# Optimization experiments

Measured on AMD Instinct MI355X. Metric: run time of the kernel, lower is better.

Reference implementation:

```python
import jax, jax.numpy as jnp
import numpy as np

N = 20000
E = 640000
C_IN = 256
C_OUT = 256
K = 2
EPS = 1e-12


def setup_inputs() -> dict:
    key = jax.random.key(0)
    k1, k2, k3, k4, k5 = jax.random.split(key, 5)
    x = jax.random.normal(k1, (N, C_IN), dtype=jnp.float32)
    edge_index = jax.random.randint(k2, (2, E), 0, N, dtype=jnp.int64)
    edge_weights = jax.random.uniform(k3, (E,), dtype=jnp.float32)
    lin_w = jax.random.normal(k4, (C_OUT, C_IN), dtype=jnp.float32) / np.sqrt(C_IN)
    lin_b = jax.random.normal(k5, (C_OUT,), dtype=jnp.float32) * 0.01
    return {"x": x, "edge_index": edge_index, "edge_weights": edge_weights,
            "lin_w": lin_w, "lin_b": lin_b}


def reference(x, edge_index, edge_weights, lin_w, lin_b):
    row, col = edge_index[0], edge_index[1]  # source -> target

    # F.normalize(x, p=2, dim=-1)
    nrm = jnp.sqrt(jnp.sum(x * x, axis=-1, keepdims=True))
    x = x / jnp.maximum(nrm, EPS)

    # gcn_norm with add_self_loops=False (PyG): deg over target nodes
    deg = jax.ops.segment_sum(edge_weights, col, num_segments=N)
    deg_inv_sqrt = jnp.where(deg > 0, 1.0 / jnp.sqrt(deg), 0.0)
    norm = deg_inv_sqrt[row] * edge_weights * deg_inv_sqrt[col]  # [E]

    # K-hop propagation: out[col] += norm * x[row]
    for _ in range(K):
        msgs = norm[:, None] * x[row]                     # [E, C]
        x = jax.ops.segment_sum(msgs, col, num_segments=N)

    # Linear layer of SGConv
    return x @ lin_w.T + lin_b
```

## Files before the change

### kernel.cpp

```cpp
#include <hip/hip_runtime.h>
#include <hip/hip_bf16.h>

#define N_NODES 20000
#define N_EDGES 640000
#define C 256
#define S 96
#define CNTS 16

#define SCATTER_BLOCKS 2500
#define NORM_BLOCKS 10000
#define WCONV_BLOCKS 256

typedef __attribute__((ext_vector_type(8))) short short8;
typedef __attribute__((ext_vector_type(4))) float float4v;

__device__ inline unsigned short f2bf(float f) {
    unsigned u = __float_as_uint(f);
    unsigned r = (u + 0x7fffu + ((u >> 16) & 1u)) >> 16;
    return (unsigned short)r;
}
__device__ inline float bf_lo(unsigned u) { return __uint_as_float(u << 16); }
__device__ inline float bf_hi(unsigned u) { return __uint_as_float(u & 0xffff0000u); }

__global__ __launch_bounds__(256) void fused_pre_kernel(
        const int* __restrict__ ei, const float* __restrict__ w,
        const float* __restrict__ x, const float* __restrict__ lw,
        int* __restrict__ cnt, unsigned* __restrict__ csr,
        unsigned* __restrict__ xs32, unsigned short* __restrict__ Wb) {
    int b = blockIdx.x;
    int t = threadIdx.x;
    if (b < SCATTER_BLOCKS) {
        __shared__ int okw[4];
        unsigned long long m = __ballot(ei[2 * t + 1] == 0);
        if ((t & 63) == 0) okw[t >> 6] = (m == 0xFFFFFFFFFFFFFFFFull) ? 1 : 0;
        __syncthreads();
        int flag = okw[0] & okw[1] & okw[2] & okw[3];
        int e = b * 256 + t;
        int r, c;
        if (flag) { r = ei[2 * e]; c = ei[2 * (N_EDGES + e)]; }
        else      { r = ei[e];     c = ei[N_EDGES + e]; }
        int pos = atomicAdd(&cnt[c * CNTS], 1);
        if (pos < S) csr[c * S + pos] = (unsigned)r | ((unsigned)f2bf(w[e]) << 16);
    } else if (b < SCATTER_BLOCKS + NORM_BLOCKS) {
        int half = t >> 7;
        int tt = t & 127;
        int i = (b - SCATTER_BLOCKS) * 2 + half;
        float2 v = ((const float2*)x)[(size_t)i * 128 + tt];
        float ss = v.x * v.x + v.y * v.y;
        #pragma unroll
        for (int o = 32; o > 0; o >>= 1) ss += __shfl_down(ss, o, 64);
        __shared__ float wsum[4];
        if ((t & 63) == 0) wsum[t >> 6] = ss;
        __syncthreads();
        float tot = wsum[half * 2] + wsum[half * 2 + 1];
        float inv = 1.0f / fmaxf(sqrtf(tot), 1e-12f);
        xs32[(size_t)i * 128 + tt] =
            (unsigned)f2bf(v.x * inv) | ((unsigned)f2bf(v.y * inv) << 16);
    } else {
        int idx = (b - SCATTER_BLOCKS - NORM_BLOCKS) * 256 + t;
        Wb[idx] = f2bf(lw[idx]);
    }
}

__global__ void deg_dis_kernel(const unsigned* __restrict__ csr, const int* __restrict__ cnt,
                               float* __restrict__ dis) {
    int wv = threadIdx.x >> 6;
    int lane = threadIdx.x & 63;
    int i = blockIdx.x * 4 + wv;
    int n = cnt[i * CNTS];
    if (n > S) n = S;
    float s = 0.0f;
    for (int b = lane; b < n; b += 64)
        s += bf_hi(__builtin_nontemporal_load(&csr[i * S + b]));
    #pragma unroll
    for (int o = 32; o > 0; o >>= 1) s += __shfl_down(s, o, 64);
    if (lane == 0) dis[i] = (s > 0.0f) ? rsqrtf(s) : 0.0f;
}

template <int POW, int SRC_DIS>
__global__ __launch_bounds__(256) void gather_kernel(const int* __restrict__ cnt,
                                                     const unsigned* __restrict__ csr,
                                                     const float* __restrict__ dis,
                                                     const unsigned* __restrict__ in,
                                                     unsigned* __restrict__ out) {
    __shared__ int ls_all[4][S];
    __shared__ float lw_all[4][S];
    int wvi = threadIdx.x >> 6;
    int lane = threadIdx.x & 63;
    int i = blockIdx.x * 4 + wvi;
    int n = cnt[i * CNTS];
    if (n > S) n = S;
    int* ls = ls_all[wvi];
    float* lw = lw_all[wvi];
    if (lane < n) {
        unsigned p = __builtin_nontemporal_load(&csr[i * S + lane]);
        int s = (int)(p & 0xffffu);
        float wv = bf_hi(p);
        if (SRC_DIS) wv *= dis[s];
        ls[lane] = s; lw[lane] = wv;
    }
    if (lane + 64 < n) {
        unsigned p = __builtin_nontemporal_load(&csr[i * S + lane + 64]);
        int s = (int)(p & 0xffffu);
        float wv = bf_hi(p);
        if (SRC_DIS) wv *= dis[s];
        ls[lane + 64] = s; lw[lane + 64] = wv;
    }
    __builtin_amdgcn_wave_barrier();

    const uint2* inr = (const uint2*)in;
    float a0 = 0.f, a1 = 0.f, a2 = 0.f, a3 = 0.f;
    int j = 0;
    for (; j + 4 <= n; j += 4) {
        int s0 = ls[j], s1 = ls[j + 1], s2 = ls[j + 2], s3 = ls[j + 3];
        float w0 = lw[j], w1 = lw[j + 1], w2 = lw[j + 2], w3 = lw[j + 3];
        uint2 v0 = inr[(size_t)s0 * 64 + lane];
        uint2 v1 = inr[(size_t)s1 * 64 + lane];
        uint2 v2 = inr[(size_t)s2 * 64 + lane];
        uint2 v3 = inr[(size_t)s3 * 64 + lane];
        a0 += w0 * bf_lo(v0.x); a1 += w0 * bf_hi(v0.x);
        a2 += w0 * bf_lo(v0.y); a3 += w0 * bf_hi(v0.y);
        a0 += w1 * bf_lo(v1.x); a1 += w1 * bf_hi(v1.x);
        a2 += w1 * bf_lo(v1.y); a3 += w1 * bf_hi(v1.y);
        a0 += w2 * bf_lo(v2.x); a1 += w2 * bf_hi(v2.x);
        a2 += w2 * bf_lo(v2.y); a3 += w2 * bf_hi(v2.y);
        a0 += w3 * bf_lo(v3.x); a1 += w3 * bf_hi(v3.x);
        a2 += w3 * bf_lo(v3.y); a3 += w3 * bf_hi(v3.y);
    }
    for (; j < n; j++) {
        int s = ls[j]; float wv = lw[j];
        uint2 v = inr[(size_t)s * 64 + lane];
        a0 += wv * bf_lo(v.x); a1 += wv * bf_hi(v.x);
        a2 += wv * bf_lo(v.y); a3 += wv * bf_hi(v.y);
    }
    float d = dis[i];
    float sc = (POW == 2) ? d * d : d;
    unsigned long long r =
        (unsigned long long)((unsigned)f2bf(a0 * sc) | ((unsigned)f2bf(a1 * sc) << 16)) |
        ((unsigned long long)((unsigned)f2bf(a2 * sc) | ((unsigned)f2bf(a3 * sc) << 16)) << 32);
    __builtin_nontemporal_store(r, (unsigned long long*)out + (size_t)i * 64 + lane);
}

__global__ __launch_bounds__(256) void gemm_kernel(const unsigned short* __restrict__ h,
                                                   const unsigned short* __restrict__ Wb,
                                                   const float* __restrict__ b,
                                                   float* __restrict__ out) {
    int wv = threadIdx.x >> 6;
    int lane = threadIdx.x & 63;
    int m = lane & 15;
    int q = lane >> 4;
    int rowbase = blockIdx.x * 64 + wv * 16;
    int rowA = rowbase + m;
    if (rowA > N_NODES - 1) rowA = N_NODES - 1;
    float4v acc[16];
    #pragma unroll
    for (int nt = 0; nt < 16; nt++) acc[nt] = (float4v){0.f, 0.f, 0.f, 0.f};
    #pragma unroll
    for (int kt = 0; kt < 8; kt++) {
        int kb = kt * 32 + q * 8;
        short8 a = *(const short8*)(h + (size_t)rowA * C + kb);
        #pragma unroll
        for (int nt = 0; nt < 16; nt++) {
            short8 bb = *(const short8*)(Wb + (nt * 16 + m) * C + kb);
            acc[nt] = __builtin_amdgcn_mfma_f32_16x16x32_bf16(a, bb, acc[nt], 0, 0, 0);
        }
    }
    #pragma unroll
    for (int nt = 0; nt < 16; nt++) {
        int col = nt * 16 + m;
        float bias = b[col];
        #pragma unroll
        for (int r = 0; r < 4; r++) {
            int ro = rowbase + q * 4 + r;
            if (ro < N_NODES)
                __builtin_nontemporal_store(acc[nt][r] + bias, &out[(size_t)ro * C + col]);
        }
    }
}

extern "C" void kernel_launch(void* const* d_in, const int* in_sizes, int n_in,
                              void* d_out, int out_size, void* d_ws, size_t ws_size,
                              hipStream_t stream) {
    const float* x  = (const float*)d_in[0];
    const int*   ei = (const int*)d_in[1];
    const float* w  = (const float*)d_in[2];
    const float* lw = (const float*)d_in[3];
    const float* lb = (const float*)d_in[4];
    float* out = (float*)d_out;

    char* ws = (char*)d_ws;
    size_t off = 0;
    auto alloc = [&](size_t bytes) -> void* {
        void* p = ws + off;
        off = (off + bytes + 255) & ~(size_t)255;
        return p;
    };
    unsigned* bufA   = (unsigned*)alloc((size_t)N_NODES * 128 * 4);
    unsigned* bufB   = (unsigned*)alloc((size_t)N_NODES * 128 * 4);
    float* dis       = (float*)alloc((size_t)N_NODES * 4);
    int*   cnt       = (int*)alloc((size_t)N_NODES * CNTS * 4);
    unsigned* csr    = (unsigned*)alloc((size_t)N_NODES * S * 4);
    unsigned short* Wb = (unsigned short*)alloc((size_t)C * C * 2);
    (void)ws_size; (void)in_sizes; (void)n_in; (void)out_size;

    hipMemsetAsync(cnt, 0, (size_t)N_NODES * CNTS * 4, stream);

    fused_pre_kernel<<<SCATTER_BLOCKS + NORM_BLOCKS + WCONV_BLOCKS, 256, 0, stream>>>(
        ei, w, x, lw, cnt, csr, bufA, Wb);
    deg_dis_kernel<<<N_NODES / 4, 256, 0, stream>>>(csr, cnt, dis);
    gather_kernel<2, 1><<<N_NODES / 4, 256, 0, stream>>>(cnt, csr, dis, bufA, bufB);
    gather_kernel<1, 0><<<N_NODES / 4, 256, 0, stream>>>(cnt, csr, dis, bufB, bufA);
    gemm_kernel<<<(N_NODES + 63) / 64, 256, 0, stream>>>(
        (const unsigned short*)bufA, Wb, lb, out);
}
```

Baseline: 224.5 us.

## Split feature columns into chunks and gather multiple edges per wave

Feature buffers are stored column-chunked (4 chunks of 64 channels) so each gather wave handles one node and one chunk, launching four times as many waves. Each wave processes 8 edges at once with 16-byte loads over a 128-byte row slice, then reduces across lane groups with xor shuffles. The aim is a smaller working set per chunk for better L2 locality and more memory parallelism. The cost is that the CSR and degree setup is repeated for every chunk, plus extra shuffle reductions and padded edge slots.

```diff
diff --git a/kernel.cpp b/kernel.cpp
--- a/kernel.cpp
+++ b/kernel.cpp
@@ -4,6 +4,8 @@
 #define N_NODES 20000
 #define N_EDGES 640000
 #define C 256
+#define CW 64
+#define NCHUNK 4
 #define S 96
 #define CNTS 16
 
@@ -54,7 +56,9 @@
         __syncthreads();
         float tot = wsum[half * 2] + wsum[half * 2 + 1];
         float inv = 1.0f / fmaxf(sqrtf(tot), 1e-12f);
-        xs32[(size_t)i * 128 + tt] =
+        int c = tt >> 5;
+        int off = tt & 31;
+        xs32[((size_t)c * N_NODES + i) * 32 + off] =
             (unsigned)f2bf(v.x * inv) | ((unsigned)f2bf(v.y * inv) << 16);
     } else {
         int idx = (b - SCATTER_BLOCKS - NORM_BLOCKS) * 256 + t;
@@ -77,7 +81,7 @@
     if (lane == 0) dis[i] = (s > 0.0f) ? rsqrtf(s) : 0.0f;
 }
 
-template <int POW, int SRC_DIS>
+template <int POW, int SRC_DIS, int OUT_CHUNKED>
 __global__ __launch_bounds__(256) void gather_kernel(const int* __restrict__ cnt,
                                                      const unsigned* __restrict__ csr,
                                                      const float* __restrict__ dis,
@@ -87,58 +91,82 @@
     __shared__ float lw_all[4][S];
     int wvi = threadIdx.x >> 6;
     int lane = threadIdx.x & 63;
-    int i = blockIdx.x * 4 + wvi;
+    int wv_id = blockIdx.x * 4 + wvi;
+    int c = wv_id / N_NODES;
+    int i = wv_id - c * N_NODES;
+    int* ls = ls_all[wvi];
+    float* lw = lw_all[wvi];
+
     int n = cnt[i * CNTS];
     if (n > S) n = S;
-    int* ls = ls_all[wvi];
-    float* lw = lw_all[wvi];
-    if (lane < n) {
-        unsigned p = __builtin_nontemporal_load(&csr[i * S + lane]);
-        int s = (int)(p & 0xffffu);
-        float wv = bf_hi(p);
-        if (SRC_DIS) wv *= dis[s];
-        ls[lane] = s; lw[lane] = wv;
-    }
-    if (lane + 64 < n) {
-        unsigned p = __builtin_nontemporal_load(&csr[i * S + lane + 64]);
-        int s = (int)(p & 0xffffu);
-        float wv = bf_hi(p);
-        if (SRC_DIS) wv *= dis[s];
-        ls[lane + 64] = s; lw[lane + 64] = wv;
+    int npad = (n + 7) & ~7;
+
+    if (lane < npad) {
+        if (lane < n) {
+            unsigned p = __builtin_nontemporal_load(&csr[i * S + lane]);
+            int s = (int)(p & 0xffffu);
+            float wv = bf_hi(p);
+            if (SRC_DIS) wv *= dis[s];
+            ls[lane] = s; lw[lane] = wv;
+        } else { ls[lane] = 0; lw[lane] = 0.0f; }
+    }
+    if (lane + 64 < npad) {
+        if (lane + 64 < n) {
+            unsigned p = __builtin_nontemporal_load(&csr[i * S + lane + 64]);
+            int s = (int)(p & 0xffffu);
+            float wv = bf_hi(p);
+            if (SRC_DIS) wv *= dis[s];
+            ls[lane + 64] = s; lw[lane + 64] = wv;
+        } else { ls[lane + 64] = 0; lw[lane + 64] = 0.0f; }
     }
     __builtin_amdgcn_wave_barrier();
 
-    const uint2* inr = (const uint2*)in;
-    float a0 = 0.f, a1 = 0.f, a2 = 0.f, a3 = 0.f;
+    int g = lane >> 3;
+    int p = lane & 7;
+    const uint4* sl4 = (const uint4*)in + (size_t)c * N_NODES * 8;
+    float a0 = 0.f, a1 = 0.f, a2 = 0.f, a3 = 0.f, a4 = 0.f, a5 = 0.f, a6 = 0.f, a7 = 0.f;
+
     int j = 0;
-    for (; j + 4 <= n; j += 4) {
-        int s0 = ls[j], s1 = ls[j + 1], s2 = ls[j + 2], s3 = ls[j + 3];
-        float w0 = lw[j], w1 = lw[j + 1], w2 = lw[j + 2], w3 = lw[j + 3];
-        uint2 v0 = inr[(size_t)s0 * 64 + lane];
-        uint2 v1 = inr[(size_t)s1 * 64 + lane];
-        uint2 v2 = inr[(size_t)s2 * 64 + lane];
-        uint2 v3 = inr[(size_t)s3 * 64 + lane];
-        a0 += w0 * bf_lo(v0.x); a1 += w0 * bf_hi(v0.x);
-        a2 += w0 * bf_lo(v0.y); a3 += w0 * bf_hi(v0.y);
-        a0 += w1 * bf_lo(v1.x); a1 += w1 * bf_hi(v1.x);
-        a2 += w1 * bf_lo(v1.y); a3 += w1 * bf_hi(v1.y);
-        a0 += w2 * bf_lo(v2.x); a1 += w2 * bf_hi(v2.x);
-        a2 += w2 * bf_lo(v2.y); a3 += w2 * bf_hi(v2.y);
-        a0 += w3 * bf_lo(v3.x); a1 += w3 * bf_hi(v3.x);
-        a2 += w3 * bf_lo(v3.y); a3 += w3 * bf_hi(v3.y);
-    }
-    for (; j < n; j++) {
-        int s = ls[j]; float wv = lw[j];
-        uint2 v = inr[(size_t)s * 64 + lane];
+    for (; j + 32 <= npad; j += 32) {
+        #pragma unroll
+        for (int u = 0; u < 4; u++) {
+            int e = j + u * 8 + g;
+            int s = ls[e]; float wv = lw[e];
+            uint4 v = sl4[(size_t)s * 8 + p];
+            a0 += wv * bf_lo(v.x); a1 += wv * bf_hi(v.x);
+            a2 += wv * bf_lo(v.y); a3 += wv * bf_hi(v.y);
+            a4 += wv * bf_lo(v.z); a5 += wv * bf_hi(v.z);
+            a6 += wv * bf_lo(v.w); a7 += wv * bf_hi(v.w);
+        }
+    }
+    for (; j < npad; j += 8) {
+        int e = j + g;
+        int s = ls[e]; float wv = lw[e];
+        uint4 v = sl4[(size_t)s * 8 + p];
         a0 += wv * bf_lo(v.x); a1 += wv * bf_hi(v.x);
         a2 += wv * bf_lo(v.y); a3 += wv * bf_hi(v.y);
-    }
-    float d = dis[i];
-    float sc = (POW == 2) ? d * d : d;
-    unsigned long long r =
-        (unsigned long long)((unsigned)f2bf(a0 * sc) | ((unsigned)f2bf(a1 * sc) << 16)) |
-        ((unsigned long long)((unsigned)f2bf(a2 * sc) | ((unsigned)f2bf(a3 * sc) << 16)) << 32);
-    __builtin_nontemporal_store(r, (unsigned long long*)out + (size_t)i * 64 + lane);
+        a4 += wv * bf_lo(v.z); a5 += wv * bf_hi(v.z);
+        a6 += wv * bf_lo(v.w); a7 += wv * bf_hi(v.w);
+    }
+
+    #pragma unroll
+    for (int off = 8; off <= 32; off <<= 1) {
+        a0 += __shfl_xor(a0, off, 64); a1 += __shfl_xor(a1, off, 64);
+        a2 += __shfl_xor(a2, off, 64); a3 += __shfl_xor(a3, off, 64);
+        a4 += __shfl_xor(a4, off, 64); a5 += __shfl_xor(a5, off, 64);
+        a6 += __shfl_xor(a6, off, 64); a7 += __shfl_xor(a7, off, 64);
+    }
+    if (g == 0) {
+        float d = dis[i];
+        float sc = (POW == 2) ? d * d : d;
+        uint4 r;
+        r.x = (unsigned)f2bf(a0 * sc) | ((unsigned)f2bf(a1 * sc) << 16);
+        r.y = (unsigned)f2bf(a2 * sc) | ((unsigned)f2bf(a3 * sc) << 16);
+        r.z = (unsigned)f2bf(a4 * sc) | ((unsigned)f2bf(a5 * sc) << 16);
+        r.w = (unsigned)f2bf(a6 * sc) | ((unsigned)f2bf(a7 * sc) << 16);
+        if (OUT_CHUNKED) ((uint4*)out)[(size_t)c * N_NODES * 8 + (size_t)i * 8 + p] = r;
+        else             ((uint4*)out)[(size_t)i * 32 + c * 8 + p] = r;
+    }
 }
 
 __global__ __launch_bounds__(256) void gemm_kernel(const unsigned short* __restrict__ h,
@@ -208,8 +236,10 @@
     fused_pre_kernel<<<SCATTER_BLOCKS + NORM_BLOCKS + WCONV_BLOCKS, 256, 0, stream>>>(
         ei, w, x, lw, cnt, csr, bufA, Wb);
     deg_dis_kernel<<<N_NODES / 4, 256, 0, stream>>>(csr, cnt, dis);
-    gather_kernel<2, 1><<<N_NODES / 4, 256, 0, stream>>>(cnt, csr, dis, bufA, bufB);
-    gather_kernel<1, 0><<<N_NODES / 4, 256, 0, stream>>>(cnt, csr, dis, bufB, bufA);
+    gather_kernel<2, 1, 1><<<NCHUNK * N_NODES / 4, 256, 0, stream>>>(
+        cnt, csr, dis, bufA, bufB);
+    gather_kernel<1, 0, 0><<<NCHUNK * N_NODES / 4, 256, 0, stream>>>(
+        cnt, csr, dis, bufB, bufA);
     gemm_kernel<<<(N_NODES + 63) / 64, 256, 0, stream>>>(
         (const unsigned short*)bufA, Wb, lb, out);
 }
```

Measured after the change: 239.4 us. 1.07x slower.
